# Kernel tuning notes

Measured on AMD Instinct MI355X. Metric: run time of the kernel, lower is better.

## Reference

```python
import jax, jax.numpy as jnp
import numpy as np
from jax import lax

P = 16        # patch_size
F = 4         # fourier_freq
E = 8         # num_experts
G = 8         # groupnorm groups = min(8, out_channel)
CIN = 128
COUT = 128
EPS = 1e-5


def conv2d(x, w):
    # x: [B,C,H,W], w: [O,I,kh,kw], stride 1, SAME padding
    return lax.conv_general_dilated(x, w, (1, 1), 'SAME',
                                    dimension_numbers=('NCHW', 'OIHW', 'NCHW'))


def group_norm(x, g, b):
    B, C, H, W = x.shape
    xg = x.reshape(B, G, C // G, H, W)
    m = xg.mean(axis=(2, 3, 4), keepdims=True)
    v = xg.var(axis=(2, 3, 4), keepdims=True)
    xn = ((xg - m) * lax.rsqrt(v + EPS)).reshape(B, C, H, W)
    return xn * g[None, :, None, None] + b[None, :, None, None]


def silu(x):
    return x * jax.nn.sigmoid(x)


def fourier_feats(Hp, Wp):
    # Fourier positional encoding of patch centers -> [Hp, Wp, 4F] (= gate_channel)
    cy = (jnp.arange(Hp, dtype=jnp.float32) + 0.5) / Hp
    cx = (jnp.arange(Wp, dtype=jnp.float32) + 0.5) / Wp
    freqs = (2.0 ** jnp.arange(F, dtype=jnp.float32)) * jnp.pi
    ay = cy[:, None] * freqs[None, :]            # [Hp, F]
    ax = cx[:, None] * freqs[None, :]            # [Wp, F]
    fy = jnp.concatenate([jnp.sin(ay), jnp.cos(ay)], axis=-1)  # [Hp, 2F]
    fx = jnp.concatenate([jnp.sin(ax), jnp.cos(ax)], axis=-1)  # [Wp, 2F]
    return jnp.concatenate([
        jnp.broadcast_to(fy[:, None, :], (Hp, Wp, 2 * F)),
        jnp.broadcast_to(fx[None, :, :], (Hp, Wp, 2 * F)),
    ], axis=-1)


def setup_inputs() -> dict:
    key = jax.random.key(0)
    ks = jax.random.split(key, 5)
    B, H, W = 8, 128, 128
    x = jax.random.normal(ks[0], (B, CIN, H, W), dtype=jnp.float32)
    expert_w = jax.random.normal(ks[1], (E, COUT, CIN, 3, 3), dtype=jnp.float32) * 0.02
    expert_g = jnp.ones((E, COUT), dtype=jnp.float32)
    expert_b = jnp.zeros((E, COUT), dtype=jnp.float32)
    router_w = jax.random.normal(ks[2], (4 * F, E), dtype=jnp.float32) * 0.1
    router_b = jnp.zeros((E,), dtype=jnp.float32)
    merge_g = jnp.ones((COUT,), dtype=jnp.float32)
    merge_b = jnp.zeros((COUT,), dtype=jnp.float32)
    gamma = jnp.ones((1,), dtype=jnp.float32) * 0.01
    post_w = jax.random.normal(ks[3], (COUT, COUT, 3, 3), dtype=jnp.float32) * 0.02
    post_g = jnp.ones((COUT,), dtype=jnp.float32)
    post_b = jnp.zeros((COUT,), dtype=jnp.float32)
    return {'x': x, 'expert_w': expert_w, 'expert_g': expert_g, 'expert_b': expert_b,
            'router_w': router_w, 'router_b': router_b, 'merge_g': merge_g,
            'merge_b': merge_b, 'gamma': gamma, 'post_w': post_w,
            'post_g': post_g, 'post_b': post_b}


def reference(x, expert_w, expert_g, expert_b, router_w, router_b,
              merge_g, merge_b, gamma, post_w, post_g, post_b):
    B, C, H, W = x.shape
    Hp, Wp = H // P, W // P

    # RouterGate: positional Fourier features -> per-patch expert weights
    feats = fourier_feats(Hp, Wp)                       # [Hp, Wp, 4F]
    logits = feats @ router_w + router_b                # [Hp, Wp, E]
    wts = jax.nn.softmax(logits, axis=-1)               # [Hp, Wp, E]

    # ConvExperts: conv3x3 -> GN -> SiLU + residual, vmapped over experts
    def expert(w, g, b):
        return silu(group_norm(conv2d(x, w), g, b)) + x

    outs = jax.vmap(expert)(expert_w, expert_g, expert_b)  # [E, B, C, H, W]

    # Broadcast patch weights to pixel resolution and merge
    wmap = jnp.repeat(jnp.repeat(wts, P, axis=0), P, axis=1)  # [H, W, E]
    merged = jnp.einsum('ebchw,hwe->bchw', outs, wmap)        # [B, C, H, W]

    # merge GN + SiLU, gamma-scaled residual
    y = x + gamma[0] * silu(group_norm(merged, merge_g, merge_b))

    # post block: conv3x3 (no bias) -> GN -> SiLU
    out = silu(group_norm(conv2d(y, post_w), post_g, post_b))
    return out
```

## Files before the change

kernel.cpp:

```cpp
#include <hip/hip_runtime.h>
#include <hip/hip_bf16.h>


typedef __attribute__((ext_vector_type(8))) short bf16x8;
typedef __attribute__((ext_vector_type(4))) float f32x4;
typedef __attribute__((ext_vector_type(2))) float f32x2;
typedef __attribute__((ext_vector_type(8))) unsigned short u16x8;
typedef __attribute__((ext_vector_type(4))) unsigned short u16x4;
typedef __attribute__((ext_vector_type(2))) unsigned int u32x2;
typedef __attribute__((ext_vector_type(2))) int i32x2;
typedef __attribute__((ext_vector_type(4))) int i32x4;
typedef __attribute__((ext_vector_type(8))) int i32x8;

__device__ __forceinline__ float b2f(unsigned short u) {
  unsigned int v = ((unsigned int)u) << 16;
  return __builtin_bit_cast(float, v);
}
__device__ __forceinline__ unsigned short f2b(float f) {
  __hip_bfloat16 h = __float2bfloat16(f);
  return __builtin_bit_cast(unsigned short, h);
}
__device__ __forceinline__ float fsilu(float x) {
  float e = __expf(-x);
  return x * __builtin_amdgcn_rcpf(1.f + e);
}
__device__ __forceinline__ void gll16(const void* g, void* l) {
  __builtin_amdgcn_global_load_lds(
      (const __attribute__((address_space(1))) unsigned int*)g,
      (__attribute__((address_space(3))) unsigned int*)l, 16, 0, 0);
}
__device__ __forceinline__ unsigned char f2fp8(float v) {
  return (unsigned char)(__builtin_amdgcn_cvt_pk_fp8_f32(v, v, 0, false) & 0xff);
}

__global__ void k_router(const float* __restrict__ rw, const float* __restrict__ rb,
                         float* __restrict__ wts) {
  int t = threadIdx.x;
  if (t >= 64) return;
  int py = t >> 3, px = t & 7;
  float cy = (py + 0.5f) / 8.f, cx = (px + 0.5f) / 8.f;
  const float PI = 3.14159265358979323846f;
  float f[16];
#pragma unroll
  for (int k = 0; k < 4; ++k) {
    float fr = (float)(1 << k) * PI;
    f[k] = sinf(cy * fr); f[4 + k] = cosf(cy * fr);
    f[8 + k] = sinf(cx * fr); f[12 + k] = cosf(cx * fr);
  }
  float lg[8], mx = -1e30f;
#pragma unroll
  for (int e = 0; e < 8; ++e) {
    float a = rb[e];
#pragma unroll
    for (int k = 0; k < 16; ++k) a += f[k] * rw[k * 8 + e];
    lg[e] = a; mx = fmaxf(mx, a);
  }
  float s = 0.f;
#pragma unroll
  for (int e = 0; e < 8; ++e) { lg[e] = __expf(lg[e] - mx); s += lg[e]; }
  float inv = 1.f / s;
#pragma unroll
  for (int e = 0; e < 8; ++e) wts[t * 8 + e] = lg[e] * inv;
}

__global__ void k_zborder(unsigned short* __restrict__ xpu,
                          unsigned char* __restrict__ xp8) {
  int idx = blockIdx.x * 256 + threadIdx.x;
  if (idx >= 8 * 516) return;
  int b = idx / 516, pxi = idx - b * 516;
  int r, c;
  if (pxi < 130)      { r = 0;   c = pxi; }
  else if (pxi < 260) { r = 129; c = pxi - 130; }
  else if (pxi < 388) { r = pxi - 260 + 1; c = 0; }
  else                { r = pxi - 388 + 1; c = 129; }
  size_t pix = (size_t)(b * 130 + r) * 130 + c;
  unsigned short* p = xpu + pix * 128;
#pragma unroll
  for (int j = 0; j < 16; ++j) *(u16x8*)(p + j * 8) = (u16x8)0;
  f32x4* q = (f32x4*)(xp8 + pix * 128);
#pragma unroll
  for (int j = 0; j < 8; ++j) q[j] = (f32x4)0.f;
}

__global__ void k_build_xpad(const float* __restrict__ x, __hip_bfloat16* __restrict__ xp,
                             unsigned char* __restrict__ xp8) {
  int bx = blockIdx.x;
  int wb = bx & 1, cib = (bx >> 1) & 1;
  int h = (bx >> 2) & 127, b = bx >> 9;
  int w0 = wb * 64, ci0 = cib * 64;
  __shared__ float t[64][65];
  int tid = threadIdx.x;
#pragma unroll
  for (int r = 0; r < 16; ++r) {
    int idx = r * 256 + tid;
    int i = idx >> 6, j = idx & 63;
    t[i][j] = x[(((size_t)b * 128 + ci0 + i) * 128 + h) * 128 + w0 + j];
  }
  __syncthreads();
  unsigned short* xpu = (unsigned short*)xp;
#pragma unroll
  for (int r = 0; r < 2; ++r) {
    int s = r * 256 + tid;
    int px = s >> 3, cg = s & 7;
    int wpad = w0 + px + 1;
    size_t pixbase = ((size_t)b * 130 + h + 1) * 130 + wpad;
    float v[8];
    u16x8 bv;
#pragma unroll
    for (int k = 0; k < 8; ++k) { v[k] = t[cg * 8 + k][px]; bv[k] = f2b(v[k]); }
    int ci = ci0 + cg * 8;
    *(u16x8*)(xpu + pixbase * 128 + ci) = bv;
    int c_phys = ((ci >> 4) + wpad) & 7;
    int pk0 = __builtin_amdgcn_cvt_pk_fp8_f32(v[0], v[1], 0, false);
    pk0 = __builtin_amdgcn_cvt_pk_fp8_f32(v[2], v[3], pk0, true);
    int pk1 = __builtin_amdgcn_cvt_pk_fp8_f32(v[4], v[5], 0, false);
    pk1 = __builtin_amdgcn_cvt_pk_fp8_f32(v[6], v[7], pk1, true);
    i32x2 pk = {pk0, pk1};
    *(i32x2*)(xp8 + pixbase * 128 + c_phys * 16 + (ci & 8)) = pk;
  }
}

__global__ void k_build_w(const float* __restrict__ src, __hip_bfloat16* __restrict__ dst) {
  int o = blockIdx.x * 256 + threadIdx.x;
  if (o >= 147456) return;
  int cl = o & 31, co = (o >> 5) & 127;
  int r9 = o >> 12;
  int tp = r9 % 9, cc = r9 / 9;
  int ci = cc * 32 + cl;
  ((unsigned short*)dst)[o] = f2b(src[((size_t)co * 128 + ci) * 9 + tp]);
}

__global__ void k_build_w8(const float* __restrict__ src, unsigned char* __restrict__ dst) {
  int o = blockIdx.x * 256 + threadIdx.x;
  if (o >= 1179648) return;
  int e = o / 147456;
  int r = o - e * 147456;
  int tap = r >> 14;
  int rr = r & 16383;
  int co = rr >> 7, byte = rr & 127;
  int c_phys = byte >> 4, j = byte & 15;
  int c_log = (c_phys - co) & 7;
  int ci = c_log * 16 + j;
  dst[o] = f2fp8(src[(((size_t)e * 128 + co) * 128 + ci) * 9 + tap]);
}

template <int G>
__global__ __launch_bounds__(512, 2) void k_conv8(
    const unsigned char* __restrict__ xp8, const unsigned char* __restrict__ wt8,
    unsigned char* __restrict__ out8base, float* __restrict__ partials) {
  __shared__ __align__(16) char smem[99328];
  const int cpx = (G * 512) >> 3;
  const int nid = (blockIdx.x & 7) * cpx + (blockIdx.x >> 3);
  const int eg = nid & (G - 1);
  const int t0 = nid / G;
  const int b = t0 >> 6, rp = t0 & 63, h0 = rp * 2;
  const unsigned char* wt = wt8 + (size_t)eg * 147456;
  unsigned char* out8 = out8base + (size_t)eg * 16777216ull;

  const int tid = threadIdx.x;
  const int lane = tid & 63, wid = tid >> 6;
  const int wm = wid >> 1, wn = wid & 1;
  const int rl = lane & 15, kg = lane >> 4;
  const int rowA = wm >> 1;
  const int colA = (wm & 1) * 64;

  int aoff[3][4][2], boff[4][2];
#pragma unroll
  for (int mb = 0; mb < 4; ++mb) {
    int col = colA + mb * 16 + rl;
#pragma unroll
    for (int kx = 0; kx < 3; ++kx) {
      int px = col + kx;
      int base = rowA * 16640 + px * 128;
      aoff[kx][mb][0] = base + ((2 * kg + px) & 7) * 16;
      aoff[kx][mb][1] = base + ((2 * kg + 1 + px) & 7) * 16;
    }
  }
#pragma unroll
  for (int nb = 0; nb < 4; ++nb) {
    int co = wn * 64 + nb * 16 + rl;
    boff[nb][0] = 66560 + co * 128 + ((2 * kg + co) & 7) * 16;
    boff[nb][1] = 66560 + co * 128 + ((2 * kg + 1 + co) & 7) * 16;
  }

  f32x4 acc[4][4] = {};

#define STGA(bi, ky_)                                                          \
  {                                                                            \
    const unsigned char* abase =                                               \
        xp8 + (size_t)(b * 130 + h0 + (ky_)) * 16640;                          \
    char* D = smem + (bi) * 33280;                                             \
    _Pragma("unroll")                                                          \
    for (int it = 0; it < 4; ++it)                                             \
      gll16(abase + (it * 512 + tid) * 16, D + (it * 512 + tid) * 16);         \
    if (tid < 32) gll16(abase + (2048 + tid) * 16, D + (2048 + tid) * 16);     \
  }
#define STGB(bi, t_)                                                           \
  {                                                                            \
    const unsigned char* bbase = wt + (t_) * 16384;                            \
    char* D = smem + 66560 + (bi) * 16384;                                     \
    gll16(bbase + tid * 16, D + tid * 16);                                     \
    gll16(bbase + (512 + tid) * 16, D + (512 + tid) * 16);                     \
  }

  STGA(0, 0);
  STGB(0, 0);
#pragma unroll
  for (int t = 0; t < 9; ++t) {
    const int ky = t / 3, kx = t % 3;
    __syncthreads();
    if (t + 1 < 9) STGB((t + 1) & 1, t + 1);
    if (kx == 0 && ky < 2) STGA((ky + 1) & 1, ky + 1);
    const char* Al = smem + (ky & 1) * 33280;
    const int bsel = (t & 1) * 16384;
    i32x8 av[4], bv[4];
#pragma unroll
    for (int mb = 0; mb < 4; ++mb) {
      i32x4 lo = *(const i32x4*)(Al + aoff[kx][mb][0]);
      i32x4 hi = *(const i32x4*)(Al + aoff[kx][mb][1]);
      av[mb][0] = lo[0]; av[mb][1] = lo[1]; av[mb][2] = lo[2]; av[mb][3] = lo[3];
      av[mb][4] = hi[0]; av[mb][5] = hi[1]; av[mb][6] = hi[2]; av[mb][7] = hi[3];
    }
#pragma unroll
    for (int nb = 0; nb < 4; ++nb) {
      i32x4 lo = *(const i32x4*)(smem + bsel + boff[nb][0]);
      i32x4 hi = *(const i32x4*)(smem + bsel + boff[nb][1]);
      bv[nb][0] = lo[0]; bv[nb][1] = lo[1]; bv[nb][2] = lo[2]; bv[nb][3] = lo[3];
      bv[nb][4] = hi[0]; bv[nb][5] = hi[1]; bv[nb][6] = hi[2]; bv[nb][7] = hi[3];
    }
#pragma unroll
    for (int mb = 0; mb < 4; ++mb)
#pragma unroll
      for (int nb = 0; nb < 4; ++nb)
        acc[mb][nb] = __builtin_amdgcn_mfma_scale_f32_16x16x128_f8f6f4(
            bv[nb], av[mb], acc[mb][nb], 0, 0,
            0, 0x7F7F7F7F, 0, 0x7F7F7F7F);
  }
#undef STGA
#undef STGB

  float sv[4] = {0, 0, 0, 0}, qv[4] = {0, 0, 0, 0};
#pragma unroll
  for (int mb = 0; mb < 4; ++mb) {
    int px = colA + mb * 16 + rl;
    int h = h0 + rowA;
    size_t base = (((size_t)b * 128 + h) * 128 + px) * 128;
#pragma unroll
    for (int nb = 0; nb < 4; ++nb) {
      int co0 = wn * 64 + nb * 16 + kg * 4;
      f32x4 v = acc[mb][nb];
#pragma unroll
      for (int j = 0; j < 4; ++j) { sv[nb] += v[j]; qv[nb] += v[j] * v[j]; }
      int pk = __builtin_amdgcn_cvt_pk_fp8_f32(v[0], v[1], 0, false);
      pk = __builtin_amdgcn_cvt_pk_fp8_f32(v[2], v[3], pk, true);
      *(int*)(out8 + base + co0) = pk;
    }
  }
  __syncthreads();
  float* sg = (float*)smem;
  if (tid < 16) sg[tid] = 0.f;
  __syncthreads();
#pragma unroll
  for (int nb = 0; nb < 4; ++nb) {
    float a = sv[nb], q = qv[nb];
#pragma unroll
    for (int o = 32; o > 0; o >>= 1) { a += __shfl_down(a, o); q += __shfl_down(q, o); }
    if (lane == 0) {
      int g = wn * 4 + nb;
      atomicAdd(&sg[g * 2 + 0], a);
      atomicAdd(&sg[g * 2 + 1], q);
    }
  }
  __syncthreads();
  if (tid < 16)
    partials[((size_t)(eg * 8 + b) * 64 + rp) * 16 + tid] = sg[tid];
}

__global__ __launch_bounds__(512, 2) void k_conv(
    const unsigned short* __restrict__ xpu, const unsigned short* __restrict__ wtu,
    unsigned short* __restrict__ outu, float* __restrict__ partials) {
  __shared__ __align__(16) char smem[90112];
  const int nid = (blockIdx.x & 7) * 64 + (blockIdx.x >> 3);
  const int b = nid >> 6, rp = nid & 63, h0 = rp * 2;
  const int tid = threadIdx.x;
  const int lane = tid & 63, wid = tid >> 6;
  const int wm = wid >> 1, wn = wid & 1;
  const int rl = lane & 15, kg = lane >> 4;
  const int rowA = wm >> 1;
  const int colA = (wm & 1) * 64;

  int aoff[3][4], boff[3][4];
#pragma unroll
  for (int mb = 0; mb < 4; ++mb) {
    int col = colA + mb * 16 + rl;
#pragma unroll
    for (int kx = 0; kx < 3; ++kx) {
      int px = col + kx;
      aoff[kx][mb] = (rowA * 160 + px) * 64 + (kg ^ ((px >> 1) & 3)) * 16;
    }
  }
#pragma unroll
  for (int kx = 0; kx < 3; ++kx)
#pragma unroll
    for (int nb = 0; nb < 4; ++nb) {
      int co = wn * 64 + nb * 16 + rl;
      boff[kx][nb] = 20480 + ((kx * 128 + co) * 4 + (kg ^ ((co >> 1) & 3))) * 16;
    }

  int soff[6];
  bool isA[6];
#pragma unroll
  for (int it = 0; it < 6; ++it) {
    int s = it * 512 + tid;
    if (s < 1280) {
      int rw = (s >= 640) ? 1 : 0;
      int off = s - rw * 640;
      int px = off >> 2, q = off & 3;
      int qg = q ^ ((px >> 1) & 3);
      isA[it] = true;
      soff[it] = rw * 33280 + px * 256 + qg * 16;
    } else {
      int s2 = s - 1280;
      int tap = s2 >> 9, r3 = s2 & 511;
      int co = r3 >> 2, q = r3 & 3;
      int qg = q ^ ((co >> 1) & 3);
      isA[it] = false;
      soff[it] = tap * 8192 + co * 64 + qg * 16;
    }
  }

  f32x4 acc[4][4] = {};
  const char* xpb = (const char*)xpu;
  const char* wtb = (const char*)wtu;

#define STAGE(bi, u)                                                           \
  {                                                                            \
    const int cc_ = (u) / 3, ky_ = (u) % 3;                                    \
    char* D = smem + (bi) * 45056;                                             \
    const char* abase =                                                        \
        xpb + (size_t)(b * 130 + h0 + ky_) * 33280 + cc_ * 64;                 \
    const char* bbase = wtb + cc_ * 73728 + ky_ * 24576;                       \
    _Pragma("unroll")                                                          \
    for (int it = 0; it < 5; ++it)                                             \
      gll16((isA[it] ? abase : bbase) + soff[it], D + (it * 512 + tid) * 16);  \
    if (tid < 256) gll16(bbase + soff[5], D + (5 * 512 + tid) * 16);           \
  }

  STAGE(0, 0);
  for (int u = 0; u < 12; ++u) {
    const int cur = u & 1;
    __syncthreads();
    if (u + 1 < 12) STAGE(cur ^ 1, u + 1);
    const char* Al = smem + cur * 45056;
#pragma unroll
    for (int kx = 0; kx < 3; ++kx) {
      bf16x8 aF[4], bF[4];
#pragma unroll
      for (int mb = 0; mb < 4; ++mb) aF[mb] = *(const bf16x8*)(Al + aoff[kx][mb]);
#pragma unroll
      for (int nb = 0; nb < 4; ++nb) bF[nb] = *(const bf16x8*)(Al + boff[kx][nb]);
#pragma unroll
      for (int mb = 0; mb < 4; ++mb)
#pragma unroll
        for (int nb = 0; nb < 4; ++nb)
          acc[mb][nb] = __builtin_amdgcn_mfma_f32_16x16x32_bf16(
              bF[nb], aF[mb], acc[mb][nb], 0, 0, 0);
    }
  }
#undef STAGE

  float sv[4] = {0, 0, 0, 0}, qv[4] = {0, 0, 0, 0};
#pragma unroll
  for (int mb = 0; mb < 4; ++mb) {
    int px = colA + mb * 16 + rl;
    int h = h0 + rowA;
    size_t base = (((size_t)b * 128 + h) * 128 + px) * 128;
#pragma unroll
    for (int nb = 0; nb < 4; ++nb) {
      int co0 = wn * 64 + nb * 16 + kg * 4;
      u16x4 pk;
#pragma unroll
      for (int j = 0; j < 4; ++j) {
        float v = acc[mb][nb][j];
        pk[j] = f2b(v);
        sv[nb] += v; qv[nb] += v * v;
      }
      *(u16x4*)(outu + base + co0) = pk;
    }
  }
  __syncthreads();
  float* sg = (float*)smem;
  if (tid < 16) sg[tid] = 0.f;
  __syncthreads();
#pragma unroll
  for (int nb = 0; nb < 4; ++nb) {
    float a = sv[nb], q = qv[nb];
#pragma unroll
    for (int o = 32; o > 0; o >>= 1) { a += __shfl_down(a, o); q += __shfl_down(q, o); }
    if (lane == 0) {
      int g = wn * 4 + nb;
      atomicAdd(&sg[g * 2 + 0], a);
      atomicAdd(&sg[g * 2 + 1], q);
    }
  }
  __syncthreads();
  if (tid < 16) partials[(size_t)nid * 16 + tid] = sg[tid];
}

__global__ void k_redstats(const float* __restrict__ partials, float* __restrict__ stats,
                           int nper) {
  int set = blockIdx.x;
  const float* p = partials + (size_t)set * 8 * nper * 16;
  float* st = stats + set * 128;
  int t = threadIdx.x;
  int o = t >> 2, j = t & 3;
  int b = o >> 4, slot = o & 15;
  int chunk = nper >> 2;
  float s = 0.f;
  for (int i = j * chunk; i < (j + 1) * chunk; ++i)
    s += p[((size_t)b * nper + i) * 16 + slot];
  s += __shfl_xor(s, 1);
  s += __shfl_xor(s, 2);
  if (j == 0) st[o] = s;
}

__global__ void k_redstats2(const float* __restrict__ p2, float* __restrict__ st) {
  int o = blockIdx.x;
  int b = o >> 4, slot = o & 15;
  float s = 0.f;
  for (int i = threadIdx.x; i < 1024; i += 256)
    s += p2[((size_t)b * 1024 + i) * 16 + slot];
#pragma unroll
  for (int off = 32; off > 0; off >>= 1) s += __shfl_down(s, off);
  __shared__ float wsm[4];
  int lane = threadIdx.x & 63, wv = threadIdx.x >> 6;
  if (lane == 0) wsm[wv] = s;
  __syncthreads();
  if (threadIdx.x == 0) st[o] = wsm[0] + wsm[1] + wsm[2] + wsm[3];
}

template <int NEXP>
__global__ void k_merge(const unsigned char* __restrict__ c0,
                        const unsigned char* __restrict__ c1,
                        const unsigned char* __restrict__ c2,
                        const unsigned char* __restrict__ c3,
                        const float* __restrict__ st, const float* __restrict__ eg,
                        const float* __restrict__ eb, const float* __restrict__ wts,
                        unsigned short* __restrict__ merged,
                        const unsigned short* __restrict__ xp,
                        float* __restrict__ partials2, int e0, int flags) {
  __shared__ float sg[16];
  int tid = threadIdx.x;
  if (tid < 16) sg[tid] = 0.f;
  __syncthreads();
  size_t idx = ((size_t)blockIdx.x * 256 + tid) * 8;
  int co0 = (int)(idx & 127);
  size_t pix = idx >> 7;
  int w = (int)(pix & 127), h = (int)((pix >> 7) & 127), b = (int)(pix >> 14);
  int g = co0 >> 4;
  const float cnt = 16.f * 128.f * 128.f;
  int patch = (h >> 4) * 8 + (w >> 4);
  const unsigned char* cs[4] = {c0, c1, c2, c3};
  float a[8] = {0, 0, 0, 0, 0, 0, 0, 0};
#pragma unroll
  for (int k = 0; k < NEXP; ++k) {
    int e = e0 + k;
    float mean = st[e * 128 + (b * 8 + g) * 2] / cnt;
    float var = st[e * 128 + (b * 8 + g) * 2 + 1] / cnt - mean * mean;
    float rstd = rsqrtf(var + 1e-5f);
    float we = wts[patch * 8 + e];
    f32x4 g0 = *(const f32x4*)(eg + e * 128 + co0);
    f32x4 g1 = *(const f32x4*)(eg + e * 128 + co0 + 4);
    f32x4 b0 = *(const f32x4*)(eb + e * 128 + co0);
    f32x4 b1 = *(const f32x4*)(eb + e * 128 + co0 + 4);
    u32x2 cv = *(const u32x2*)(cs[k] + idx);
    f32x2 d0 = __builtin_amdgcn_cvt_pk_f32_fp8(cv[0], false);
    f32x2 d1 = __builtin_amdgcn_cvt_pk_f32_fp8(cv[0], true);
    f32x2 d2 = __builtin_amdgcn_cvt_pk_f32_fp8(cv[1], false);
    f32x2 d3 = __builtin_amdgcn_cvt_pk_f32_fp8(cv[1], true);
    float d[8] = {d0[0], d0[1], d1[0], d1[1], d2[0], d2[1], d3[0], d3[1]};
#pragma unroll
    for (int i = 0; i < 8; ++i) {
      float gi = (i < 4) ? g0[i] : g1[i - 4];
      float bi = (i < 4) ? b0[i] : b1[i - 4];
      float A = rstd * gi;
      float B = bi - mean * A;
      a[i] += we * fsilu(d[i] * A + B);
    }
  }
  if (flags & 1) {
    u16x8 mv = *(const u16x8*)(merged + idx);
#pragma unroll
    for (int i = 0; i < 8; ++i) a[i] += b2f(mv[i]);
  }
  u16x8 out;
  float s = 0.f, q = 0.f;
  if (flags & 2) {
    const unsigned short* xr =
        xp + (((size_t)b * 130 + h + 1) * 130 + (w + 1)) * 128 + co0;
    u16x8 xv = *(const u16x8*)xr;
#pragma unroll
    for (int i = 0; i < 8; ++i) {
      a[i] += b2f(xv[i]);
      out[i] = f2b(a[i]);
      float rv = b2f(out[i]);
      s += rv; q += rv * rv;
    }
  } else {
#pragma unroll
    for (int i = 0; i < 8; ++i) out[i] = f2b(a[i]);
  }
  *(u16x8*)(merged + idx) = out;
  if (flags & 2) {
    atomicAdd(&sg[g * 2 + 0], s);
    atomicAdd(&sg[g * 2 + 1], q);
    __syncthreads();
    if (tid < 16) partials2[(size_t)blockIdx.x * 16 + tid] = sg[tid];
  }
}

__global__ void k_ypass(const unsigned short* __restrict__ merged,
                        unsigned short* __restrict__ xp,
                        const float* __restrict__ st, const float* __restrict__ mg,
                        const float* __restrict__ mbv, const float* __restrict__ gptr) {
  size_t idx = ((size_t)blockIdx.x * 256 + threadIdx.x) * 8;
  int co0 = (int)(idx & 127);
  size_t pix = idx >> 7;
  int w = (int)(pix & 127), h = (int)((pix >> 7) & 127), b = (int)(pix >> 14);
  int g = co0 >> 4;
  const float cnt = 16.f * 128.f * 128.f;
  float mean = st[(b * 8 + g) * 2] / cnt;
  float var = st[(b * 8 + g) * 2 + 1] / cnt - mean * mean;
  float rstd = rsqrtf(var + 1e-5f);
  float gm = gptr[0];
  unsigned short* xr = xp + (((size_t)b * 130 + h + 1) * 130 + (w + 1)) * 128 + co0;
  u16x8 xv = *(const u16x8*)xr;
  u16x8 mv = *(const u16x8*)(merged + idx);
  u16x8 yv;
#pragma unroll
  for (int i = 0; i < 8; ++i) {
    float xf = b2f(xv[i]);
    float M = b2f(mv[i]);
    float xn = (M - mean) * rstd * mg[co0 + i] + mbv[co0 + i];
    yv[i] = f2b(xf + gm * fsilu(xn));
  }
  *(u16x8*)xr = yv;
}

__global__ void k_final(const __hip_bfloat16* __restrict__ conv, const float* __restrict__ st,
                        const float* __restrict__ pg, const float* __restrict__ pb,
                        float* __restrict__ out) {
  int bx = blockIdx.x;
  int wb = bx & 1, h = (bx >> 1) & 127, b = bx >> 8;
  int w0 = wb * 64;
  __shared__ float t[64][129];
  int tid = threadIdx.x;
  const float cnt = 16.f * 128.f * 128.f;
  const unsigned short* cu = (const unsigned short*)conv;
#pragma unroll
  for (int r = 0; r < 32; ++r) {
    int e2 = r * 256 + tid;
    int co = e2 & 127, wl = e2 >> 7;
    int g = co >> 4;
    float mean = st[(b * 8 + g) * 2] / cnt;
    float var = st[(b * 8 + g) * 2 + 1] / cnt - mean * mean;
    float rstd = rsqrtf(var + 1e-5f);
    float v = b2f(cu[(((size_t)b * 128 + h) * 128 + w0 + wl) * 128 + co]);
    float xn = (v - mean) * rstd * pg[co] + pb[co];
    t[wl][co] = fsilu(xn);
  }
  __syncthreads();
#pragma unroll
  for (int r = 0; r < 8; ++r) {
    int f = r * 256 + tid;
    int jb = f & 15, co = f >> 4;
    f32x4 o;
#pragma unroll
    for (int j = 0; j < 4; ++j) o[j] = t[jb * 4 + j][co];
    *(f32x4*)&out[(((size_t)b * 128 + co) * 128 + h) * 128 + w0 + jb * 4] = o;
  }
}

extern "C" void kernel_launch(void* const* d_in, const int* in_sizes, int n_in,
                              void* d_out, int out_size, void* d_ws, size_t ws_size,
                              hipStream_t stream) {
  const float* x        = (const float*)d_in[0];
  const float* expert_w = (const float*)d_in[1];
  const float* expert_g = (const float*)d_in[2];
  const float* expert_b = (const float*)d_in[3];
  const float* router_w = (const float*)d_in[4];
  const float* router_b = (const float*)d_in[5];
  const float* merge_g  = (const float*)d_in[6];
  const float* merge_b  = (const float*)d_in[7];
  const float* gamma    = (const float*)d_in[8];
  const float* post_w   = (const float*)d_in[9];
  const float* post_g   = (const float*)d_in[10];
  const float* post_b   = (const float*)d_in[11];

  char* ws = (char*)d_ws;
  float* wts            = (float*)(ws + 0);
  float* stats          = (float*)(ws + 2048);
  float* partials       = (float*)(ws + 8192);
  float* partials2      = (float*)(ws + 270336);
  unsigned short* wtbp  = (unsigned short*)(ws + 794624);
  unsigned char* wtb8   = (unsigned char*)(ws + 1089536);
  unsigned short* xpad  = (unsigned short*)(ws + 2269184);
  unsigned char* xpad8  = (unsigned char*)(ws + 36888576);
  const size_t BUFS = 54198272ull;
  const size_t FB = 16777216ull;
  const size_t NEED2 = BUFS + 2 * FB + 33554432ull;
  const size_t NEED4 = BUFS + 4 * FB + 33554432ull;
  int nbuf = (ws_size >= NEED4) ? 4 : 2;
  unsigned char* bufs0 = (unsigned char*)(ws + BUFS);
  unsigned short* merged = (unsigned short*)(ws + BUFS + (size_t)nbuf * FB);
  unsigned short* pbuf = (unsigned short*)(ws + BUFS);
  if (ws_size < NEED2) {
    hipMemsetAsync(d_out, 0, (size_t)out_size * 4, stream);
    return;
  }

  k_zborder<<<17, 256, 0, stream>>>(xpad, xpad8);
  k_router<<<1, 64, 0, stream>>>(router_w, router_b, wts);
  k_build_xpad<<<4096, 256, 0, stream>>>(x, (__hip_bfloat16*)xpad, xpad8);
  k_build_w<<<576, 256, 0, stream>>>(post_w, (__hip_bfloat16*)wtbp);
  k_build_w8<<<4608, 256, 0, stream>>>(expert_w, wtb8);

  if (nbuf == 4) {
    for (int p = 0; p < 2; ++p) {
      k_conv8<4><<<2048, 512, 0, stream>>>(xpad8, wtb8 + (size_t)(p * 4) * 147456,
                                           bufs0, partials);
      k_redstats<<<4, 512, 0, stream>>>(partials, stats + p * 4 * 128, 64);
      int flags = (p > 0 ? 1 : 0) | (p == 1 ? 2 : 0);
      k_merge<4><<<8192, 256, 0, stream>>>(bufs0, bufs0 + FB, bufs0 + 2 * FB,
                                           bufs0 + 3 * FB, stats, expert_g, expert_b,
                                           wts, merged, xpad, partials2, p * 4, flags);
    }
  } else {
    for (int p = 0; p < 4; ++p) {
      k_conv8<2><<<1024, 512, 0, stream>>>(xpad8, wtb8 + (size_t)(p * 2) * 147456,
                                           bufs0, partials);
      k_redstats<<<2, 512, 0, stream>>>(partials, stats + p * 2 * 128, 64);
      int flags = (p > 0 ? 1 : 0) | (p == 3 ? 2 : 0);
      k_merge<2><<<8192, 256, 0, stream>>>(bufs0, bufs0 + FB, bufs0, bufs0 + FB,
                                           stats, expert_g, expert_b, wts, merged,
                                           xpad, partials2, p * 2, flags);
    }
  }
  k_redstats2<<<128, 256, 0, stream>>>(partials2, stats + 8 * 128);
  k_ypass<<<8192, 256, 0, stream>>>(merged, xpad, stats + 8 * 128, merge_g, merge_b, gamma);
  k_conv<<<512, 512, 0, stream>>>(xpad, wtbp, pbuf, partials);
  k_redstats<<<1, 512, 0, stream>>>(partials, stats + 9 * 128, 64);
  k_final<<<2048, 256, 0, stream>>>((const __hip_bfloat16*)pbuf, stats + 9 * 128,
                                    post_g, post_b, (float*)d_out);
}
```

Before: 402.8 us.

## Load expert conv weights straight to registers and stage all input rows once

The fp8 expert conv kernel stops staging weights through LDS. Each lane now reads its own weight fragment from global memory into double-buffered registers, and the weight layout drops its swizzle to match. All four input rows are loaded into LDS once up front, which removes the per-tap __syncthreads and the double-buffered A stages. This frees LDS and barriers but makes weight loads uncoalesced and exposes their latency to global memory, and launch bounds drop to one block per CU, raising register pressure.

```diff
diff --git a/kernel.cpp b/kernel.cpp
--- a/kernel.cpp
+++ b/kernel.cpp
@@ -137,18 +137,15 @@
   int r = o - e * 147456;
   int tap = r >> 14;
   int rr = r & 16383;
-  int co = rr >> 7, byte = rr & 127;
-  int c_phys = byte >> 4, j = byte & 15;
-  int c_log = (c_phys - co) & 7;
-  int ci = c_log * 16 + j;
+  int co = rr >> 7, ci = rr & 127;
   dst[o] = f2fp8(src[(((size_t)e * 128 + co) * 128 + ci) * 9 + tap]);
 }
 
 template <int G>
-__global__ __launch_bounds__(512, 2) void k_conv8(
+__global__ __launch_bounds__(512, 1) void k_conv8(
     const unsigned char* __restrict__ xp8, const unsigned char* __restrict__ wt8,
     unsigned char* __restrict__ out8base, float* __restrict__ partials) {
-  __shared__ __align__(16) char smem[99328];
+  __shared__ __align__(16) char smem[66560];
   const int cpx = (G * 512) >> 3;
   const int nid = (blockIdx.x & 7) * cpx + (blockIdx.x >> 3);
   const int eg = nid & (G - 1);
@@ -164,80 +161,74 @@
   const int rowA = wm >> 1;
   const int colA = (wm & 1) * 64;
 
-  int aoff[3][4][2], boff[4][2];
+  int aoff[3][4][2];
 #pragma unroll
   for (int mb = 0; mb < 4; ++mb) {
     int col = colA + mb * 16 + rl;
 #pragma unroll
     for (int kx = 0; kx < 3; ++kx) {
       int px = col + kx;
-      int base = rowA * 16640 + px * 128;
+      int base = px * 128;
       aoff[kx][mb][0] = base + ((2 * kg + px) & 7) * 16;
       aoff[kx][mb][1] = base + ((2 * kg + 1 + px) & 7) * 16;
     }
   }
+  int bgo[4];
+#pragma unroll
+  for (int nb = 0; nb < 4; ++nb)
+    bgo[nb] = (wn * 64 + nb * 16 + rl) * 128 + kg * 32;
+
+  {
+    const unsigned char* abase = xp8 + (size_t)(b * 130 + h0) * 16640;
+#pragma unroll
+    for (int it = 0; it < 8; ++it)
+      gll16(abase + (it * 512 + tid) * 16, smem + (it * 512 + tid) * 16);
+    if (tid < 64) gll16(abase + (4096 + tid) * 16, smem + (4096 + tid) * 16);
+  }
+
+  f32x4 acc[4][4] = {};
+  i32x4 breg[2][8];
+
 #pragma unroll
   for (int nb = 0; nb < 4; ++nb) {
-    int co = wn * 64 + nb * 16 + rl;
-    boff[nb][0] = 66560 + co * 128 + ((2 * kg + co) & 7) * 16;
-    boff[nb][1] = 66560 + co * 128 + ((2 * kg + 1 + co) & 7) * 16;
-  }
-
-  f32x4 acc[4][4] = {};
-
-#define STGA(bi, ky_)                                                          \
-  {                                                                            \
-    const unsigned char* abase =                                               \
-        xp8 + (size_t)(b * 130 + h0 + (ky_)) * 16640;                          \
-    char* D = smem + (bi) * 33280;                                             \
-    _Pragma("unroll")                                                          \
-    for (int it = 0; it < 4; ++it)                                             \
-      gll16(abase + (it * 512 + tid) * 16, D + (it * 512 + tid) * 16);         \
-    if (tid < 32) gll16(abase + (2048 + tid) * 16, D + (2048 + tid) * 16);     \
-  }
-#define STGB(bi, t_)                                                           \
-  {                                                                            \
-    const unsigned char* bbase = wt + (t_) * 16384;                            \
-    char* D = smem + 66560 + (bi) * 16384;                                     \
-    gll16(bbase + tid * 16, D + tid * 16);                                     \
-    gll16(bbase + (512 + tid) * 16, D + (512 + tid) * 16);                     \
-  }
-
-  STGA(0, 0);
-  STGB(0, 0);
+    const unsigned char* p = wt + bgo[nb];
+    breg[0][nb * 2] = *(const i32x4*)p;
+    breg[0][nb * 2 + 1] = *(const i32x4*)(p + 16);
+  }
+
+  __syncthreads();
+
 #pragma unroll
   for (int t = 0; t < 9; ++t) {
+    if (t + 1 < 9) {
+      const unsigned char* bb = wt + (t + 1) * 16384;
+#pragma unroll
+      for (int nb = 0; nb < 4; ++nb) {
+        const unsigned char* p = bb + bgo[nb];
+        breg[(t + 1) & 1][nb * 2] = *(const i32x4*)p;
+        breg[(t + 1) & 1][nb * 2 + 1] = *(const i32x4*)(p + 16);
+      }
+    }
     const int ky = t / 3, kx = t % 3;
-    __syncthreads();
-    if (t + 1 < 9) STGB((t + 1) & 1, t + 1);
-    if (kx == 0 && ky < 2) STGA((ky + 1) & 1, ky + 1);
-    const char* Al = smem + (ky & 1) * 33280;
-    const int bsel = (t & 1) * 16384;
-    i32x8 av[4], bv[4];
+    const char* Ar = smem + (rowA + ky) * 16640;
+    i32x8 av[4];
 #pragma unroll
     for (int mb = 0; mb < 4; ++mb) {
-      i32x4 lo = *(const i32x4*)(Al + aoff[kx][mb][0]);
-      i32x4 hi = *(const i32x4*)(Al + aoff[kx][mb][1]);
-      av[mb][0] = lo[0]; av[mb][1] = lo[1]; av[mb][2] = lo[2]; av[mb][3] = lo[3];
-      av[mb][4] = hi[0]; av[mb][5] = hi[1]; av[mb][6] = hi[2]; av[mb][7] = hi[3];
+      i32x4 lo = *(const i32x4*)(Ar + aoff[kx][mb][0]);
+      i32x4 hi = *(const i32x4*)(Ar + aoff[kx][mb][1]);
+      av[mb] = __builtin_shufflevector(lo, hi, 0, 1, 2, 3, 4, 5, 6, 7);
     }
 #pragma unroll
     for (int nb = 0; nb < 4; ++nb) {
-      i32x4 lo = *(const i32x4*)(smem + bsel + boff[nb][0]);
-      i32x4 hi = *(const i32x4*)(smem + bsel + boff[nb][1]);
-      bv[nb][0] = lo[0]; bv[nb][1] = lo[1]; bv[nb][2] = lo[2]; bv[nb][3] = lo[3];
-      bv[nb][4] = hi[0]; bv[nb][5] = hi[1]; bv[nb][6] = hi[2]; bv[nb][7] = hi[3];
-    }
-#pragma unroll
-    for (int mb = 0; mb < 4; ++mb)
-#pragma unroll
-      for (int nb = 0; nb < 4; ++nb)
+      i32x8 bv = __builtin_shufflevector(breg[t & 1][nb * 2], breg[t & 1][nb * 2 + 1],
+                                         0, 1, 2, 3, 4, 5, 6, 7);
+#pragma unroll
+      for (int mb = 0; mb < 4; ++mb)
         acc[mb][nb] = __builtin_amdgcn_mfma_scale_f32_16x16x128_f8f6f4(
-            bv[nb], av[mb], acc[mb][nb], 0, 0,
+            bv, av[mb], acc[mb][nb], 0, 0,
             0, 0x7F7F7F7F, 0, 0x7F7F7F7F);
-  }
-#undef STGA
-#undef STGB
+    }
+  }
 
   float sv[4] = {0, 0, 0, 0}, qv[4] = {0, 0, 0, 0};
 #pragma unroll
```

Result: slower. 544.7 us (+35.2%).
